# Optimization experiments

Measured on AMD Instinct MI355X. Metric: run time of the kernel, lower is better.

## Reference

```python
import jax, jax.numpy as jnp
import numpy as np

EPS = 1e-5

def _bn(x, p):
    # eval-mode BatchNorm over the last (channel) axis; p = [gamma, beta, mean, var]
    g, b, m, v = p[0], p[1], p[2], p[3]
    return (x - m) * jax.lax.rsqrt(v + EPS) * g + b

def _mk_bn(key, c):
    kg, kb, km, kv = jax.random.split(key, 4)
    return jnp.stack([
        jax.random.uniform(kg, (c,), minval=0.5, maxval=1.5),
        jax.random.normal(kb, (c,)) * 0.1,
        jax.random.normal(km, (c,)) * 0.1,
        jax.random.uniform(kv, (c,), minval=0.5, maxval=1.5),
    ]).astype(jnp.float32)

def setup_inputs() -> dict:
    key = jax.random.key(0)
    ks = jax.random.split(key, 12)
    B, N, K = 2, 65536, 16
    IN_CH, OUT_CH = 32, 128
    D = IN_CH + 3            # 35
    C16 = OUT_CH // 16       # 8
    C4 = OUT_CH // 4         # 32
    G = 1                    # num_group
    feats = jax.random.normal(ks[0], (B, N, D), dtype=jnp.float32)
    idx = jax.random.randint(ks[1], (B, N, K), 0, N, dtype=jnp.int64)
    s = lambda fi, fo: (2.0 / fi) ** 0.5
    return {
        "features": feats,
        "idx": idx,
        "point_W": jax.random.normal(ks[2], (10, C16), dtype=jnp.float32) * s(10, C16),
        "point_bn": _mk_bn(ks[3], C16),
        "eta_W": jax.random.normal(ks[4], (IN_CH, C16), dtype=jnp.float32) * s(IN_CH, C16),
        "eta_bn": _mk_bn(ks[5], C16),
        "mu_W": jax.random.normal(ks[6], (IN_CH, C16), dtype=jnp.float32) * s(IN_CH, C16),
        "mu_bn": _mk_bn(ks[7], C16),
        "gamma_W": jax.random.normal(ks[8], (D, C4), dtype=jnp.float32) * s(D, C4),
        "gamma_bn": _mk_bn(ks[9], C4),
        "map_W": jax.random.normal(ks[10], (3 * C16, G), dtype=jnp.float32) * s(3 * C16, G),
        "map_bn": _mk_bn(ks[10], G),
        "fc_W": jax.random.normal(ks[11], (C4, OUT_CH), dtype=jnp.float32) * s(C4, OUT_CH),
    }

def reference(features, idx, point_W, point_bn, eta_W, eta_bn, mu_W, mu_bn,
              gamma_W, gamma_bn, map_W, map_bn, fc_W):
    # features: [B,N,D] (D = 3 xyz + in_channel), idx: [B,N,K] kNN indices
    nbr = jax.vmap(lambda f, i: f[i])(features, idx)     # [B,N,K,D] gather
    pn = nbr[..., :3]                                    # neighbor xyz
    pnf = nbr[..., 3:]                                   # neighbor feats
    feat = features[..., 3:]                             # center feats [B,N,Cin]
    p = features[:, :, None, :3]                         # center xyz, bcast over K
    diff = p - pn
    point = jnp.concatenate([
        jnp.sum(diff * diff, axis=-1, keepdims=True),
        jnp.broadcast_to(p, pn.shape), pn, diff,
    ], axis=-1)                                          # [B,N,K,10]
    point = jax.nn.relu(_bn(point @ point_W, point_bn))  # [B,N,K,C16]
    eta = _bn((feat @ eta_W)[:, :, None, :], eta_bn)     # [B,N,1,C16] (repeat over K)
    mu = _bn(pnf @ mu_W, mu_bn)                          # [B,N,K,C16]
    feature = jnp.concatenate([jnp.broadcast_to(eta, mu.shape), mu], axis=-1)  # concat mode
    feature = jnp.concatenate([point, feature], axis=-1)                       # [B,N,K,3*C16]
    feature = jax.nn.relu(_bn(feature @ map_W, map_bn))  # [B,N,K,G]
    gam = _bn(nbr @ gamma_W, gamma_bn)                   # [B,N,K,C4]
    rep = gam.shape[-1] // feature.shape[-1]             # out/4 / num_group
    feature = jnp.tile(feature, (1, 1, 1, rep))          # channel repeat
    out = jnp.max(feature * gam, axis=2)                 # max over neighbors -> [B,N,C4]
    return out @ fc_W                                    # [B,N,out_channel]
```

## Files before the change

kernel.cpp:

```cpp
#include <hip/hip_runtime.h>
#include <hip/hip_fp16.h>
#include <math.h>

#define N_PTS   65536
#define BATCH   2
#define TOTAL   (BATCH * N_PTS)
#define NPACK_DW 16
#define CPACK   12
#define EPSB    1e-5f

typedef float  f32x4  __attribute__((ext_vector_type(4)));
typedef _Float16 f16x8 __attribute__((ext_vector_type(8)));

static __device__ inline unsigned h2u(float a, float b) {
    __half2 h = __floats2half2_rn(a, b);
    union { __half2 h; unsigned u; } cv; cv.h = h; return cv.u;
}
static __device__ inline float2 u2f2(unsigned u) {
    union { unsigned u; __half2 h; } cv; cv.u = u; return __half22float2(cv.h);
}
static __device__ inline unsigned pk_max(unsigned a, unsigned b) {
    unsigned r; asm("v_pk_max_f16 %0, %1, %2" : "=v"(r) : "v"(a), "v"(b)); return r;
}
static __device__ inline unsigned pk_fma(unsigned a, unsigned b, unsigned c) {
    unsigned r; asm("v_pk_fma_f16 %0, %1, %2, %3" : "=v"(r) : "v"(a), "v"(b), "v"(c)); return r;
}
static __device__ inline unsigned pkrtz(float a, float b) {
    unsigned r; asm("v_cvt_pkrtz_f16_f32 %0, %1, %2" : "=v"(r) : "v"(a), "v"(b)); return r;
}

__global__ __launch_bounds__(256) void k1_precompute(
    const float* __restrict__ feats,
    const float* __restrict__ pW,
    const float* __restrict__ pBN,
    const float* __restrict__ eW,
    const float* __restrict__ eBN,
    const float* __restrict__ mW,
    const float* __restrict__ mBN,
    const float* __restrict__ gW,
    const float* __restrict__ gBN,
    const float* __restrict__ mapW,
    const float* __restrict__ mapBN,
    const float* __restrict__ fcW,
    unsigned* __restrict__ packN,
    float* __restrict__ packC,
    unsigned* __restrict__ fc16,
    float* __restrict__ gateC)
{
    __shared__ __align__(16) unsigned char sPk[4][1792];

    const int tid  = threadIdx.x;
    const int lane = tid & 63, wv = tid >> 6;
    const int lm   = lane & 15, lq = lane >> 4;
    const int pt0  = blockIdx.x * 64 + wv * 16;

    f16x8 bG0, bG1, bEM;
    {
        union { unsigned short u[8]; f16x8 v; } c0, c1, c2;
#pragma unroll
        for (int j = 0; j < 8; ++j) {
            const int k = 8 * lq + j;
            c0.u[j] = __half_as_ushort(__float2half_rn(gW[(3 + k) * 32 + lm]));
            c1.u[j] = __half_as_ushort(__float2half_rn(gW[(3 + k) * 32 + 16 + lm]));
            const float w2 = (lm < 8) ? eW[k * 8 + lm] : mW[k * 8 + (lm - 8)];
            c2.u[j] = __half_as_ushort(__float2half_rn(w2));
        }
        bG0 = c0.v; bG1 = c1.v; bEM = c2.v;
    }
    const float sA = gBN[lm]      / sqrtf(gBN[96 + lm]  + EPSB);
    const float tA = gBN[32 + lm] - gBN[64 + lm] * sA;
    const float sB = gBN[16 + lm] / sqrtf(gBN[112 + lm] + EPSB);
    const float tB = gBN[48 + lm] - gBN[80 + lm] * sB;
    const float w0a = gW[lm],      w1a = gW[32 + lm],      w2a = gW[64 + lm];
    const float w0b = gW[16 + lm], w1b = gW[48 + lm],      w2b = gW[80 + lm];
    float sE_, tE_, mpw;
    if (lm < 8) {
        sE_ = eBN[lm] / sqrtf(eBN[24 + lm] + EPSB);
        tE_ = eBN[8 + lm] - eBN[16 + lm] * sE_;
        mpw = mapW[8 + lm];
    } else {
        const int qq = lm - 8;
        sE_ = mBN[qq] / sqrtf(mBN[24 + qq] + EPSB);
        tE_ = mBN[8 + qq] - mBN[16 + qq] * sE_;
        mpw = mapW[16 + qq];
    }
    const int  q   = lm & 7;
    const bool isB = lm < 8;
    const float pw0 = pW[q];
    const float sp  = pBN[q] / sqrtf(pBN[24 + q] + EPSB);
    const float tp  = pBN[8 + q] - pBN[16 + q] * sp;
    float cxx, cyy, czz;
    if (isB) { cxx = pW[32+q]-pW[56+q]; cyy = pW[40+q]-pW[64+q]; czz = pW[48+q]-pW[72+q]; }
    else     { cxx = pW[8+q] +pW[56+q]; cyy = pW[16+q]+pW[64+q]; czz = pW[24+q]+pW[72+q]; }

    f16x8 afrag;
    {
        const float* ar = feats + (size_t)(pt0 + lm) * 35 + 3 + 8 * lq;
        const float4 a0 = *(const float4*)ar;
        const float4 a1 = *(const float4*)(ar + 4);
        union { unsigned u[4]; f16x8 v; } cv;
        cv.u[0] = h2u(a0.x, a0.y); cv.u[1] = h2u(a0.z, a0.w);
        cv.u[2] = h2u(a1.x, a1.y); cv.u[3] = h2u(a1.z, a1.w);
        afrag = cv.v;
    }
    float X[4], Y[4], Z[4], PP[4];
#pragma unroll
    for (int r = 0; r < 4; ++r) {
        const float* rr = feats + (size_t)(pt0 + 4 * lq + r) * 35;
        X[r] = rr[0]; Y[r] = rr[1]; Z[r] = rr[2];
        PP[r] = X[r]*X[r] + Y[r]*Y[r] + Z[r]*Z[r];
    }

    f32x4 aG0 = {0.f,0.f,0.f,0.f}, aG1 = {0.f,0.f,0.f,0.f}, aEM = {0.f,0.f,0.f,0.f};
    aG0 = __builtin_amdgcn_mfma_f32_16x16x32_f16(afrag, bG0, aG0, 0, 0, 0);
    aG1 = __builtin_amdgcn_mfma_f32_16x16x32_f16(afrag, bG1, aG1, 0, 0, 0);
    aEM = __builtin_amdgcn_mfma_f32_16x16x32_f16(afrag, bEM, aEM, 0, 0, 0);

    float G0[4], G1[4], eD[4], mD[4], BA[4], gm[4], iv[4];
#pragma unroll
    for (int r = 0; r < 4; ++r) {
        G0[r] = fmaf(aG0[r] + X[r]*w0a + Y[r]*w1a + Z[r]*w2a, sA, tA);
        G1[r] = fmaf(aG1[r] + X[r]*w0b + Y[r]*w1b + Z[r]*w2b, sB, tB);
        float v = fmaf(aEM[r], sE_, tE_) * mpw;
        v += __shfl_xor(v, 1);
        v += __shfl_xor(v, 2);
        v += __shfl_xor(v, 4);
        const float o = __shfl_xor(v, 8);
        eD[r] = isB ? v : o;
        mD[r] = isB ? o : v;
        const float raw = PP[r]*pw0 + X[r]*cxx + Y[r]*cyy + Z[r]*czz;
        BA[r] = isB ? raw * sp : fmaf(raw, sp, tp);
        float m = fmaxf(fabsf(G0[r]), fabsf(G1[r]));
        m = fmaxf(m, __shfl_xor(m, 1));
        m = fmaxf(m, __shfl_xor(m, 2));
        m = fmaxf(m, __shfl_xor(m, 4));
        m = fmaxf(m, __shfl_xor(m, 8));
        gm[r] = m;
        iv[r] = (m > 0.f) ? (127.f / m) : 0.f;
    }

    unsigned char* PNl = sPk[wv];
    unsigned char* PCl = sPk[wv] + 1024;
    const int pos = (0x3120 >> ((lm & 3) * 4)) & 0xF;
    const int gb0 = 24 + ((lm >> 2) << 2) + pos;
#pragma unroll
    for (int r = 0; r < 4; ++r) {
        const int row = 4 * lq + r;
        unsigned char* RN = PNl + row * 64;
        RN[gb0]      = (unsigned char)((int)rintf(G0[r] * iv[r]) + 128);
        RN[gb0 + 16] = (unsigned char)((int)rintf(G1[r] * iv[r]) + 128);
        if (isB) {
            *(unsigned short*)(RN + 8 + 2 * q) =
                __half_as_ushort(__float2half_rn(BA[r]));
        } else {
            *(float*)(PCl + row * 48 + 16 + 4 * q) = BA[r];
        }
        if (lm == 0)
            *(float4*)(PCl + row * 48) = make_float4(X[r], Y[r], Z[r], eD[r]);
        if (lm == 1) {
            *(unsigned*)(RN + 0) = h2u(X[r], Y[r]);
            *(unsigned*)(RN + 4) = h2u(Z[r], mD[r]);
        }
        if (lm == 2) {
            union { float f; unsigned u; } sc; sc.f = gm[r];
            *(unsigned*)(RN + 56) = sc.u;
            *(unsigned*)(RN + 60) = 0u;
        }
    }

    {
        const uint4 v = *(const uint4*)(PNl + (lane >> 2) * 64 + (lane & 3) * 16);
        ((uint4*)packN)[(size_t)(pt0 + (lane >> 2)) * 4 + (lane & 3)] = v;
    }
    if (lane < 48) {
        const int pr = lane / 3, pc = lane % 3;
        const uint4 v = *(const uint4*)(PCl + pr * 48 + pc * 16);
        ((uint4*)packC)[(size_t)(pt0 + pr) * 3 + pc] = v;
    }

    if (blockIdx.x == 0) {
        for (int fi = tid; fi < 512; fi += 256) {
            const int flm = fi & 15, nt = (fi >> 4) & 7, flq = fi >> 7;
            unsigned dws[4];
#pragma unroll
            for (int p = 0; p < 4; ++p) {
                const float a = fcW[(8 * flq + 2 * p)     * 128 + nt * 16 + flm];
                const float b = fcW[(8 * flq + 2 * p + 1) * 128 + nt * 16 + flm];
                dws[p] = h2u(a, b);
            }
            ((uint4*)fc16)[fi] = make_uint4(dws[0], dws[1], dws[2], dws[3]);
        }
        if (tid == 0) {
#pragma unroll
            for (int qq = 0; qq < 8; ++qq) {
                const float g = pBN[qq], v = pBN[24 + qq];
                const float s = g / sqrtf(v + EPSB);
                gateC[qq]     = 2.f * pW[qq] * s;
                gateC[8 + qq] = mapW[qq];
            }
            const float g = mapBN[0], b = mapBN[1], m = mapBN[2], v = mapBN[3];
            const float ms = g / sqrtf(v + EPSB);
            gateC[16] = ms;
            gateC[17] = b - m * ms;
        }
    }
}

__global__ __launch_bounds__(256) void k2_aggregate_fc(
    const int* __restrict__ idx,
    const unsigned* __restrict__ packN,
    const float* __restrict__ packC,
    const unsigned* __restrict__ fc16,
    const float* __restrict__ gateC,
    float* __restrict__ out)
{
    __shared__ __align__(16) unsigned short sPool[32 * 40];

    const int bid  = blockIdx.x;
    const int xcd  = bid & 7, slot = bid >> 3;
    const int cb   = (xcd < 4) ? (slot * 4 + xcd)
                               : (2048 + slot * 4 + (xcd - 4));
    const int cbase = cb * 32;

    const int tid  = threadIdx.x;
    const int cl   = tid >> 3;
    const int ks   = tid & 7;
    const int c    = cbase + cl;
    const int lane = tid & 63;
    const int w    = tid >> 6;
    const int lm   = lane & 15, lq = lane >> 4;

    f16x8 bfrag[2];
#pragma unroll
    for (int ntj = 0; ntj < 2; ++ntj) {
        union { uint4 u4; f16x8 v; } cv;
        cv.u4 = ((const uint4*)fc16)[(lq * 8 + 2 * w + ntj) * 16 + lm];
        bfrag[ntj] = cv.v;
    }

    const float ms = gateC[16], mt = gateC[17];
    float W0p[8], mW0[8];
#pragma unroll
    for (int qq = 0; qq < 8; ++qq) { W0p[qq] = gateC[qq]; mW0[qq] = gateC[8 + qq]; }

    const float4* PC = (const float4*)(packC + (size_t)c * CPACK);
    const float4 c0 = PC[0], c1 = PC[1], c2 = PC[2];
    const float px = c0.x, py = c0.y, pz = c0.z, etadot = c0.w;
    const float Ap[8] = { c1.x, c1.y, c1.z, c1.w, c2.x, c2.y, c2.z, c2.w };

    const int2 ib2 = ((const int2*)idx)[c * 8 + ks];
    const int bbase = c & ~(N_PTS - 1);

    unsigned o16[16];
#pragma unroll
    for (int qq = 0; qq < 16; ++qq) o16[qq] = 0xFC00FC00u;

    const uint4* P0 = (const uint4*)(packN + (size_t)(bbase + ib2.x) * NPACK_DW);
    const uint4* P1 = (const uint4*)(packN + (size_t)(bbase + ib2.y) * NPACK_DW);
    uint4 n0[4] = { P0[0], P0[1], P0[2], P0[3] };
    uint4 n1[4] = { P1[0], P1[1], P1[2], P1[3] };

#pragma unroll
    for (int k = 0; k < 2; ++k) {
        const uint4* N = k ? n1 : n0;
        const float2 xy = u2f2(N[0].x), zM = u2f2(N[0].y);
        const float dot3 = px * xy.x + py * xy.y + pz * zM.x;

        const unsigned bn[4] = { N[0].z, N[0].w, N[1].x, N[1].y };
        float pd = 0.f;
#pragma unroll
        for (int qq = 0; qq < 4; ++qq) {
            const float2 bn2 = u2f2(bn[qq]);
            const float u0 = Ap[2 * qq]     + bn2.x - dot3 * W0p[2 * qq];
            const float u1 = Ap[2 * qq + 1] + bn2.y - dot3 * W0p[2 * qq + 1];
            pd = fmaf(fmaxf(u0, 0.f), mW0[2 * qq], pd);
            pd = fmaf(fmaxf(u1, 0.f), mW0[2 * qq + 1], pd);
        }
        float s = fmaf(pd + etadot + zM.y, ms, mt);
        s = fmaxf(s, 0.f);

        union { unsigned u; float f; } sc; sc.u = N[3].z;
        const float t = s * sc.f * (1.f / 127.f);
        const unsigned t2 = pkrtz(t, t);
        const float d = -1152.f * t;
        const unsigned d2 = pkrtz(d, d);

        const unsigned gd[8] = { N[1].z, N[1].w, N[2].x, N[2].y,
                                 N[2].z, N[2].w, N[3].x, N[3].y };
#pragma unroll
        for (int qd = 0; qd < 8; ++qd) {
            const unsigned dwv = gd[qd];
            const unsigned lo = (dwv & 0x00FF00FFu) | 0x64006400u;
            const unsigned hi = ((dwv >> 8) & 0x00FF00FFu) | 0x64006400u;
            o16[2 * qd]     = pk_max(o16[2 * qd],     pk_fma(lo, t2, d2));
            o16[2 * qd + 1] = pk_max(o16[2 * qd + 1], pk_fma(hi, t2, d2));
        }
    }

#pragma unroll
    for (int qq = 0; qq < 16; ++qq) {
        unsigned v = o16[qq];
        v = pk_max(v, (unsigned)__shfl_xor((int)v, 1));
        v = pk_max(v, (unsigned)__shfl_xor((int)v, 2));
        v = pk_max(v, (unsigned)__shfl_xor((int)v, 4));
        o16[qq] = v;
    }

    {
        uint2 pk;
        pk.x = o16[2 * ks];
        pk.y = o16[2 * ks + 1];
        *(uint2*)(sPool + cl * 40 + ks * 4) = pk;
    }
    __syncthreads();

    f32x4 acc[2][2];
#pragma unroll
    for (int a = 0; a < 2; ++a)
#pragma unroll
        for (int b = 0; b < 2; ++b)
            acc[a][b] = (f32x4){0.f, 0.f, 0.f, 0.f};

#pragma unroll
    for (int mtile = 0; mtile < 2; ++mtile) {
        const f16x8 afrag = *(const f16x8*)(sPool + (mtile * 16 + lm) * 40 + lq * 8);
#pragma unroll
        for (int ntj = 0; ntj < 2; ++ntj)
            acc[mtile][ntj] = __builtin_amdgcn_mfma_f32_16x16x32_f16(
                afrag, bfrag[ntj], acc[mtile][ntj], 0, 0, 0);
    }

#pragma unroll
    for (int mtile = 0; mtile < 2; ++mtile)
#pragma unroll
        for (int ntj = 0; ntj < 2; ++ntj) {
            const int nt = 2 * w + ntj;
#pragma unroll
            for (int r = 0; r < 4; ++r)
                __builtin_nontemporal_store(acc[mtile][ntj][r],
                    &out[(size_t)(cbase + mtile * 16 + lq * 4 + r) * 128 + nt * 16 + lm]);
        }
}

extern "C" void kernel_launch(void* const* d_in, const int* in_sizes, int n_in,
                              void* d_out, int out_size, void* d_ws, size_t ws_size,
                              hipStream_t stream) {
    const float* feats    = (const float*)d_in[0];
    const int*   idx      = (const int*)  d_in[1];
    const float* point_W  = (const float*)d_in[2];
    const float* point_bn = (const float*)d_in[3];
    const float* eta_W    = (const float*)d_in[4];
    const float* eta_bn   = (const float*)d_in[5];
    const float* mu_W     = (const float*)d_in[6];
    const float* mu_bn    = (const float*)d_in[7];
    const float* gamma_W  = (const float*)d_in[8];
    const float* gamma_bn = (const float*)d_in[9];
    const float* map_W    = (const float*)d_in[10];
    const float* map_bn   = (const float*)d_in[11];
    const float* fc_W     = (const float*)d_in[12];
    float* out = (float*)d_out;

    unsigned* packN = (unsigned*)d_ws;
    float*    packC = (float*)(packN + (size_t)TOTAL * NPACK_DW);
    unsigned* fc16  = (unsigned*)(packC + (size_t)TOTAL * CPACK);
    float*    gateC = (float*)(fc16 + 2048);

    hipLaunchKernelGGL(k1_precompute, dim3(TOTAL / 64), dim3(256), 0, stream,
                       feats, point_W, point_bn, eta_W, eta_bn, mu_W, mu_bn,
                       gamma_W, gamma_bn, map_W, map_bn, fc_W,
                       packN, packC, fc16, gateC);
    hipLaunchKernelGGL(k2_aggregate_fc, dim3(TOTAL / 32), dim3(256), 0, stream,
                       idx, packN, packC, fc16, gateC, out);
}
```

Baseline: 146.2 us.

## Stage feature tile in LDS and use per-half int8 quantization scales

The precompute kernel now loads each block's 64x35 feature tile into shared memory with coalesced float4 copies, then reads the MFMA fragments and xyz from LDS. Before, each lane did strided global loads. The int8 quantization of gamma now keeps a separate max-abs scale for each 16-channel half, stored in the formerly unused pad word. The main kernel decodes each half with its own scale and switches from round-toward-zero to round-to-nearest f16 conversion. This is mainly an accuracy improvement, at the cost of a few extra shuffles and conversions per neighbor.

```diff
diff --git a/kernel.cpp b/kernel.cpp
--- a/kernel.cpp
+++ b/kernel.cpp
@@ -24,9 +24,6 @@
 }
 static __device__ inline unsigned pk_fma(unsigned a, unsigned b, unsigned c) {
     unsigned r; asm("v_pk_fma_f16 %0, %1, %2, %3" : "=v"(r) : "v"(a), "v"(b), "v"(c)); return r;
-}
-static __device__ inline unsigned pkrtz(float a, float b) {
-    unsigned r; asm("v_cvt_pkrtz_f16_f32 %0, %1, %2" : "=v"(r) : "v"(a), "v"(b)); return r;
 }
 
 __global__ __launch_bounds__(256) void k1_precompute(
@@ -47,12 +44,19 @@
     unsigned* __restrict__ fc16,
     float* __restrict__ gateC)
 {
+    __shared__ float sF[64 * 35];
     __shared__ __align__(16) unsigned char sPk[4][1792];
 
     const int tid  = threadIdx.x;
     const int lane = tid & 63, wv = tid >> 6;
     const int lm   = lane & 15, lq = lane >> 4;
     const int pt0  = blockIdx.x * 64 + wv * 16;
+
+    {
+        const float4* src = (const float4*)(feats + (size_t)blockIdx.x * 64 * 35);
+        float4* dst = (float4*)sF;
+        for (int i = tid; i < 560; i += 256) dst[i] = src[i];
+    }
 
     f16x8 bG0, bG1, bEM;
     {
@@ -93,20 +97,20 @@
     if (isB) { cxx = pW[32+q]-pW[56+q]; cyy = pW[40+q]-pW[64+q]; czz = pW[48+q]-pW[72+q]; }
     else     { cxx = pW[8+q] +pW[56+q]; cyy = pW[16+q]+pW[64+q]; czz = pW[24+q]+pW[72+q]; }
 
+    __syncthreads();
+
     f16x8 afrag;
     {
-        const float* ar = feats + (size_t)(pt0 + lm) * 35 + 3 + 8 * lq;
-        const float4 a0 = *(const float4*)ar;
-        const float4 a1 = *(const float4*)(ar + 4);
+        const float* ar = sF + (wv * 16 + lm) * 35 + 3 + 8 * lq;
         union { unsigned u[4]; f16x8 v; } cv;
-        cv.u[0] = h2u(a0.x, a0.y); cv.u[1] = h2u(a0.z, a0.w);
-        cv.u[2] = h2u(a1.x, a1.y); cv.u[3] = h2u(a1.z, a1.w);
+        cv.u[0] = h2u(ar[0], ar[1]); cv.u[1] = h2u(ar[2], ar[3]);
+        cv.u[2] = h2u(ar[4], ar[5]); cv.u[3] = h2u(ar[6], ar[7]);
         afrag = cv.v;
     }
     float X[4], Y[4], Z[4], PP[4];
 #pragma unroll
     for (int r = 0; r < 4; ++r) {
-        const float* rr = feats + (size_t)(pt0 + 4 * lq + r) * 35;
+        const float* rr = sF + (wv * 16 + 4 * lq + r) * 35;
         X[r] = rr[0]; Y[r] = rr[1]; Z[r] = rr[2];
         PP[r] = X[r]*X[r] + Y[r]*Y[r] + Z[r]*Z[r];
     }
@@ -116,7 +120,7 @@
     aG1 = __builtin_amdgcn_mfma_f32_16x16x32_f16(afrag, bG1, aG1, 0, 0, 0);
     aEM = __builtin_amdgcn_mfma_f32_16x16x32_f16(afrag, bEM, aEM, 0, 0, 0);
 
-    float G0[4], G1[4], eD[4], mD[4], BA[4], gm[4], iv[4];
+    float G0[4], G1[4], eD[4], mD[4], BA[4], gm0[4], gm1[4], iv0[4], iv1[4];
 #pragma unroll
     for (int r = 0; r < 4; ++r) {
         G0[r] = fmaf(aG0[r] + X[r]*w0a + Y[r]*w1a + Z[r]*w2a, sA, tA);
@@ -130,13 +134,14 @@
         mD[r] = isB ? o : v;
         const float raw = PP[r]*pw0 + X[r]*cxx + Y[r]*cyy + Z[r]*czz;
         BA[r] = isB ? raw * sp : fmaf(raw, sp, tp);
-        float m = fmaxf(fabsf(G0[r]), fabsf(G1[r]));
-        m = fmaxf(m, __shfl_xor(m, 1));
-        m = fmaxf(m, __shfl_xor(m, 2));
-        m = fmaxf(m, __shfl_xor(m, 4));
-        m = fmaxf(m, __shfl_xor(m, 8));
-        gm[r] = m;
-        iv[r] = (m > 0.f) ? (127.f / m) : 0.f;
+        float m0 = fabsf(G0[r]), m1 = fabsf(G1[r]);
+        m0 = fmaxf(m0, __shfl_xor(m0, 1)); m1 = fmaxf(m1, __shfl_xor(m1, 1));
+        m0 = fmaxf(m0, __shfl_xor(m0, 2)); m1 = fmaxf(m1, __shfl_xor(m1, 2));
+        m0 = fmaxf(m0, __shfl_xor(m0, 4)); m1 = fmaxf(m1, __shfl_xor(m1, 4));
+        m0 = fmaxf(m0, __shfl_xor(m0, 8)); m1 = fmaxf(m1, __shfl_xor(m1, 8));
+        gm0[r] = m0; gm1[r] = m1;
+        iv0[r] = (m0 > 0.f) ? (127.f / m0) : 0.f;
+        iv1[r] = (m1 > 0.f) ? (127.f / m1) : 0.f;
     }
 
     unsigned char* PNl = sPk[wv];
@@ -147,8 +152,8 @@
     for (int r = 0; r < 4; ++r) {
         const int row = 4 * lq + r;
         unsigned char* RN = PNl + row * 64;
-        RN[gb0]      = (unsigned char)((int)rintf(G0[r] * iv[r]) + 128);
-        RN[gb0 + 16] = (unsigned char)((int)rintf(G1[r] * iv[r]) + 128);
+        RN[gb0]      = (unsigned char)((int)rintf(G0[r] * iv0[r]) + 128);
+        RN[gb0 + 16] = (unsigned char)((int)rintf(G1[r] * iv1[r]) + 128);
         if (isB) {
             *(unsigned short*)(RN + 8 + 2 * q) =
                 __half_as_ushort(__float2half_rn(BA[r]));
@@ -162,9 +167,9 @@
             *(unsigned*)(RN + 4) = h2u(Z[r], mD[r]);
         }
         if (lm == 2) {
-            union { float f; unsigned u; } sc; sc.f = gm[r];
-            *(unsigned*)(RN + 56) = sc.u;
-            *(unsigned*)(RN + 60) = 0u;
+            union { float f; unsigned u; } s0, s1; s0.f = gm0[r]; s1.f = gm1[r];
+            *(unsigned*)(RN + 56) = s0.u;
+            *(unsigned*)(RN + 60) = s1.u;
         }
     }
 
@@ -279,16 +284,18 @@
         float s = fmaf(pd + etadot + zM.y, ms, mt);
         s = fmaxf(s, 0.f);
 
-        union { unsigned u; float f; } sc; sc.u = N[3].z;
-        const float t = s * sc.f * (1.f / 127.f);
-        const unsigned t2 = pkrtz(t, t);
-        const float d = -1152.f * t;
-        const unsigned d2 = pkrtz(d, d);
+        union { unsigned u; float f; } s0, s1; s0.u = N[3].z; s1.u = N[3].w;
+        const float t0 = s * s0.f * (1.f / 127.f);
+        const float t1 = s * s1.f * (1.f / 127.f);
+        const unsigned t02 = h2u(t0, t0), d02 = h2u(-1152.f * t0, -1152.f * t0);
+        const unsigned t12 = h2u(t1, t1), d12 = h2u(-1152.f * t1, -1152.f * t1);
 
         const unsigned gd[8] = { N[1].z, N[1].w, N[2].x, N[2].y,
                                  N[2].z, N[2].w, N[3].x, N[3].y };
 #pragma unroll
         for (int qd = 0; qd < 8; ++qd) {
+            const unsigned t2 = (qd < 4) ? t02 : t12;
+            const unsigned d2 = (qd < 4) ? d02 : d12;
             const unsigned dwv = gd[qd];
             const unsigned lo = (dwv & 0x00FF00FFu) | 0x64006400u;
             const unsigned hi = ((dwv >> 8) & 0x00FF00FFu) | 0x64006400u;
```

After: 146.9 us. No clear change (+0.5%).
